# Kernel tuning notes

Hardware: AMD Instinct MI355X
Metric: run time of the kernel (lower is better)

The kernel has to match this reference:

```python
import jax, jax.numpy as jnp
import numpy as np

E = 1024
H = 16
EPS = 1e-5


def setup_inputs() -> dict:
    key = jax.random.key(0)
    ks = jax.random.split(key, 17)
    B, T = 8, 1024
    s = 0.02
    inp = {
        'x': jax.random.normal(ks[0], (B, T, E), dtype=jnp.float32),
        'Wq': jax.random.normal(ks[1], (E, E), dtype=jnp.float32) * s,
        'bq': jnp.zeros((E,), jnp.float32),
        'Wk': jax.random.normal(ks[2], (E, E), dtype=jnp.float32) * s,
        'bk': jnp.zeros((E,), jnp.float32),
        'Wv': jax.random.normal(ks[3], (E, E), dtype=jnp.float32) * s,
        'bv': jnp.zeros((E,), jnp.float32),
        'Wo': jax.random.normal(ks[4], (E, E), dtype=jnp.float32) * s,
        'bo': jnp.zeros((E,), jnp.float32),
        'W1': jax.random.normal(ks[5], (E, 4 * E), dtype=jnp.float32) * s,
        'b1': jnp.zeros((4 * E,), jnp.float32),
        'W2': jax.random.normal(ks[6], (4 * E, E), dtype=jnp.float32) * s,
        'b2': jnp.zeros((E,), jnp.float32),
        'g1': jnp.ones((E,), jnp.float32),
        'be1': jnp.zeros((E,), jnp.float32),
        'g2': jnp.ones((E,), jnp.float32),
        'be2': jnp.zeros((E,), jnp.float32),
    }
    return inp


def _layernorm(x, g, b):
    mu = jnp.mean(x, axis=-1, keepdims=True)
    var = jnp.mean(jnp.square(x - mu), axis=-1, keepdims=True)
    return (x - mu) * jax.lax.rsqrt(var + EPS) * g + b


def _block(x, Wq, bq, Wk, bk, Wv, bv, Wo, bo, W1, b1, W2, b2, g1, be1, g2, be2):
    B, T, Ee = x.shape
    hd = Ee // H
    q = (x @ Wq + bq).reshape(B, T, H, hd).transpose(0, 2, 1, 3)  # (B,H,T,d)
    k = (x @ Wk + bk).reshape(B, T, H, hd).transpose(0, 2, 1, 3)
    v = (x @ Wv + bv).reshape(B, T, H, hd).transpose(0, 2, 1, 3)
    scores = jnp.einsum('bhqd,bhkd->bhqk', q, k) / jnp.sqrt(jnp.float32(hd))
    causal = jnp.tril(jnp.ones((T, T), bool))
    scores = jnp.where(causal, scores, -jnp.inf)
    w = jax.nn.softmax(scores, axis=-1)
    attn = jnp.einsum('bhqk,bhkd->bhqd', w, v)
    attn = attn.transpose(0, 2, 1, 3).reshape(B, T, Ee)
    attn = attn @ Wo + bo  # dropout is identity (p=0 / eval)
    x = _layernorm(x + attn, g1, be1)
    ff = jax.nn.relu(x @ W1 + b1) @ W2 + b2
    x = _layernorm(x + ff, g2, be2)
    return x


def reference(x, Wq, bq, Wk, bk, Wv, bv, Wo, bo, W1, b1, W2, b2, g1, be1, g2, be2):
    return _block(x, Wq, bq, Wk, bk, Wv, bv, Wo, bo, W1, b1, W2, b2, g1, be1, g2, be2)
```

## Files before the change

kernel.cpp:

```cpp
#include <hip/hip_runtime.h>
#include <math.h>

typedef unsigned short u16;
typedef __attribute__((ext_vector_type(8))) short short8;
typedef __attribute__((ext_vector_type(4))) float floatx4;
typedef __attribute__((ext_vector_type(16))) float floatx16;

__device__ __forceinline__ u16 f2bf(float f) {
    unsigned u = __float_as_uint(f);
    unsigned r = u + 0x7fffu + ((u >> 16) & 1u);
    return (u16)(r >> 16);
}

__device__ __forceinline__ void gload16(const u16* g, u16* l) {
    __builtin_amdgcn_global_load_lds((const __attribute__((address_space(1))) void*)g,
                                     (__attribute__((address_space(3))) void*)l, 16, 0, 0);
}

template<int EPI>
__global__ __launch_bounds__(256) void gemm_mfma(
    const u16* __restrict__ A, const u16* __restrict__ Bt,
    const float* __restrict__ bias, const float* __restrict__ bias2,
    const float* __restrict__ bias3, const float* __restrict__ R,
    void* __restrict__ Cout, void* __restrict__ out2, void* __restrict__ out3,
    int M, int N, int K) {
    __shared__ u16 As[128 * 32];
    __shared__ u16 Bs[128 * 32];
    const int tid = threadIdx.x;
    const int wave = tid >> 6, lane = tid & 63;
    const int ar = lane & 31, hl = lane >> 5;
    const int ny = M >> 7, nx = N >> 7;
    const int per = ny * nx;
    const int chunk = blockIdx.x / per, rem = blockIdx.x % per;
    const int nchunks = gridDim.x / per;
    const int by = rem % ny, bx = rem / ny;
    const int m0 = by * 128, n0 = bx * 128;
    const int wm = (wave & 1) * 64, wn = (wave >> 1) * 64;
    const int klen = K / nchunks;
    const int kstart = chunk * klen, kend = kstart + klen;

    floatx16 acc[2][2];
#pragma unroll
    for (int i = 0; i < 2; i++)
#pragma unroll
        for (int j = 0; j < 2; j++)
#pragma unroll
            for (int r = 0; r < 16; r++) acc[i][j][r] = 0.f;

    const int f0 = wave * 128 + lane;

    for (int k0 = kstart; k0 < kend; k0 += 32) {
        __syncthreads();
#pragma unroll
        for (int i = 0; i < 2; i++) {
            int f = f0 + i * 64;
            int row = f >> 2, c = f & 3;
            int cg = c ^ ((row >> 1) & 3);
            gload16(A + (size_t)(m0 + row) * K + k0 + cg * 8, As + f * 8);
            gload16(Bt + (size_t)(n0 + row) * K + k0 + cg * 8, Bs + f * 8);
        }
        __syncthreads();
        short8 af[2][2], bf[2][2];
#pragma unroll
        for (int mt = 0; mt < 2; mt++) {
            int row = wm + mt * 32 + ar;
            int sw = (row >> 1) & 3;
#pragma unroll
            for (int s = 0; s < 2; s++) {
                int ch = (s * 2 + hl) ^ sw;
                af[mt][s] = *(const short8*)(As + row * 32 + ch * 8);
            }
        }
#pragma unroll
        for (int nt = 0; nt < 2; nt++) {
            int row = wn + nt * 32 + ar;
            int sw = (row >> 1) & 3;
#pragma unroll
            for (int s = 0; s < 2; s++) {
                int ch = (s * 2 + hl) ^ sw;
                bf[nt][s] = *(const short8*)(Bs + row * 32 + ch * 8);
            }
        }
#pragma unroll
        for (int s = 0; s < 2; s++)
#pragma unroll
            for (int mt = 0; mt < 2; mt++)
#pragma unroll
                for (int nt = 0; nt < 2; nt++)
                    acc[mt][nt] = __builtin_amdgcn_mfma_f32_32x32x16_bf16(af[mt][s], bf[nt][s], acc[mt][nt], 0, 0, 0);
    }

    const float* bp = bias;
    int sec = 0;
    if (EPI == 4) {
        sec = n0 >> 10;
        bp = sec == 0 ? bias : (sec == 1 ? bias2 : bias3);
    }
    float bv[2];
    if (EPI != 5) {
#pragma unroll
        for (int nt = 0; nt < 2; nt++) {
            int gc = n0 + wn + nt * 32 + ar;
            bv[nt] = bp[EPI == 4 ? (gc & 1023) : gc];
        }
    }

#pragma unroll
    for (int mt = 0; mt < 2; mt++)
#pragma unroll
        for (int nt = 0; nt < 2; nt++) {
            floatx16 a = acc[mt][nt];
            int gc = n0 + wn + nt * 32 + ar;
#pragma unroll
            for (int rg = 0; rg < 4; rg++) {
                int gr0 = m0 + wm + mt * 32 + rg * 8 + hl * 4;
                if (EPI == 1) {
                    u16* C = (u16*)Cout;
#pragma unroll
                    for (int rr = 0; rr < 4; rr++)
                        C[(size_t)(gr0 + rr) * N + gc] = f2bf(fmaxf(a[rg * 4 + rr] + bv[nt], 0.f));
                } else if (EPI == 2) {
                    float* C = (float*)Cout;
#pragma unroll
                    for (int rr = 0; rr < 4; rr++) {
                        size_t idx = (size_t)(gr0 + rr) * N + gc;
                        C[idx] = a[rg * 4 + rr] + bv[nt] + R[idx];
                    }
                } else if (EPI == 5) {
                    float* C = (float*)Cout;
#pragma unroll
                    for (int rr = 0; rr < 4; rr++)
                        unsafeAtomicAdd(&C[(size_t)(gr0 + rr) * N + gc], a[rg * 4 + rr]);
                } else {
                    int nc = gc & 1023;
                    if (sec < 2) {
                        u16* C = (u16*)(sec == 0 ? Cout : out2);
#pragma unroll
                        for (int rr = 0; rr < 4; rr++)
                            C[(size_t)(gr0 + rr) * 1024 + nc] = f2bf(a[rg * 4 + rr] + bv[nt]);
                    } else {
                        u16* C = (u16*)out3;
                        int bb = gr0 >> 10, t0 = gr0 & 1023;
                        size_t idx = ((size_t)(bb * 1024 + nc)) * 1024 + t0;
                        ushort4 u;
                        u.x = f2bf(a[rg * 4 + 0] + bv[nt]); u.y = f2bf(a[rg * 4 + 1] + bv[nt]);
                        u.z = f2bf(a[rg * 4 + 2] + bv[nt]); u.w = f2bf(a[rg * 4 + 3] + bv[nt]);
                        *(ushort4*)(C + idx) = u;
                    }
                }
            }
        }
}

__global__ __launch_bounds__(256) void attn_mfma(
    const u16* __restrict__ q, const u16* __restrict__ k,
    const u16* __restrict__ vT, u16* __restrict__ o) {
    __shared__ u16 Kb[2][64 * 64];
    __shared__ u16 Vb[2][64 * 64];
    __shared__ u16 Pb[4][2][16 * 72];

    const int tid = threadIdx.x;
    const int wave = tid >> 6, lane = tid & 63;
    const int lrow = lane & 15, quad = lane >> 4;
    const int qb = blockIdx.y, bh = blockIdx.x;
    const int b = bh >> 4, h = bh & 15;
    const size_t tokbase = (size_t)b * 1024;
    const int ktmax = qb * 2 + 1;

#pragma unroll
    for (int i = 0; i < 2; i++) {
        int f = wave * 128 + i * 64 + lane;
        int row = f >> 3, c = f & 7, cg = c ^ (row & 7);
        gload16(q + (tokbase + qb * 128 + row) * 1024 + h * 64 + cg * 8, Kb[1] + f * 8);
        gload16(q + (tokbase + qb * 128 + 64 + row) * 1024 + h * 64 + cg * 8, Vb[1] + f * 8);
        gload16(k + (tokbase + row) * 1024 + h * 64 + cg * 8, Kb[0] + f * 8);
        gload16(vT + (tokbase + h * 64 + row) * 1024 + cg * 8, Vb[0] + f * 8);
    }
    asm volatile("s_waitcnt vmcnt(0)" ::: "memory");
    __syncthreads();
    short8 aQ[2][2];
#pragma unroll
    for (int band = 0; band < 2; band++)
#pragma unroll
        for (int ks = 0; ks < 2; ks++) {
            int row = wave * 16 + lrow;
            int pos = (ks * 4 + quad) ^ (lrow & 7);
            const u16* src = band ? Vb[1] : Kb[1];
            aQ[band][ks] = *(const short8*)(src + row * 64 + pos * 8);
        }
    __syncthreads();

    float lp[2][4];
    floatx4 oa[2][4];
#pragma unroll
    for (int bd = 0; bd < 2; bd++)
#pragma unroll
        for (int i = 0; i < 4; i++) { lp[bd][i] = 0.f; oa[bd][i] = {0.f, 0.f, 0.f, 0.f}; }

    for (int kt = 0; kt <= ktmax; kt++) {
        const int cur = kt & 1;
        if (kt < ktmax) {
            const int nxt = cur ^ 1;
#pragma unroll
            for (int i = 0; i < 2; i++) {
                int f = wave * 128 + i * 64 + lane;
                int row = f >> 3, c = f & 7, cg = c ^ (row & 7);
                gload16(k + (tokbase + (kt + 1) * 64 + row) * 1024 + h * 64 + cg * 8, Kb[nxt] + f * 8);
                gload16(vT + (tokbase + h * 64 + row) * 1024 + (kt + 1) * 64 + cg * 8, Vb[nxt] + f * 8);
            }
        }
#pragma unroll
        for (int band = 0; band < 2; band++) {
            const int btile = qb * 2 + band;
            if (kt > btile) continue;
            floatx4 sacc[4];
#pragma unroll
            for (int nt = 0; nt < 4; nt++) sacc[nt] = {0.f, 0.f, 0.f, 0.f};
#pragma unroll
            for (int nt = 0; nt < 4; nt++)
#pragma unroll
                for (int ks = 0; ks < 2; ks++) {
                    int row = nt * 16 + lrow;
                    int pos = (ks * 4 + quad) ^ (lrow & 7);
                    short8 bK = *(const short8*)(Kb[cur] + row * 64 + pos * 8);
                    sacc[nt] = __builtin_amdgcn_mfma_f32_16x16x32_bf16(aQ[band][ks], bK, sacc[nt], 0, 0, 0);
                }
            const bool diag = (kt == btile);
            float p[4][4];
#pragma unroll
            for (int r = 0; r < 4; r++) {
                int qrl = wave * 16 + quad * 4 + r;
#pragma unroll
                for (int nt = 0; nt < 4; nt++) {
                    float e = exp2f(sacc[nt][r] * 0.18033688011112042f);
                    if (diag && (nt * 16 + lrow) > qrl) e = 0.f;
                    p[nt][r] = e;
                    lp[band][r] += e;
                }
            }
            u16* Pw = Pb[wave][band];
#pragma unroll
            for (int nt = 0; nt < 4; nt++)
#pragma unroll
                for (int r = 0; r < 4; r++) {
                    int row = quad * 4 + r, key = nt * 16 + lrow;
                    int pos = ((key >> 3) ^ (row & 7)) * 8 + (key & 7);
                    Pw[row * 72 + pos] = f2bf(p[nt][r]);
                }
            asm volatile("s_waitcnt lgkmcnt(0)" ::: "memory");
            short8 aP[2];
#pragma unroll
            for (int ks = 0; ks < 2; ks++) {
                int pos = (ks * 4 + quad) ^ (lrow & 7);
                aP[ks] = *(const short8*)(Pw + lrow * 72 + pos * 8);
            }
#pragma unroll
            for (int nt = 0; nt < 4; nt++)
#pragma unroll
                for (int ks = 0; ks < 2; ks++) {
                    int row = nt * 16 + lrow;
                    int pos = (ks * 4 + quad) ^ (lrow & 7);
                    short8 bV = *(const short8*)(Vb[cur] + row * 64 + pos * 8);
                    oa[band][nt] = __builtin_amdgcn_mfma_f32_16x16x32_bf16(aP[ks], bV, oa[band][nt], 0, 0, 0);
                }
        }
        __syncthreads();
    }

#pragma unroll
    for (int band = 0; band < 2; band++) {
        float inv[4];
#pragma unroll
        for (int r = 0; r < 4; r++) {
            float l = lp[band][r];
#pragma unroll
            for (int off = 1; off < 16; off <<= 1) l += __shfl_xor(l, off);
            inv[r] = 1.f / l;
        }
#pragma unroll
        for (int nt = 0; nt < 4; nt++)
#pragma unroll
            for (int r = 0; r < 4; r++) {
                int grow = qb * 128 + band * 64 + wave * 16 + quad * 4 + r;
                float v = oa[band][nt][r] * inv[r];
                o[(tokbase + grow) * 1024 + h * 64 + nt * 16 + lrow] = f2bf(v);
            }
    }
}

__device__ __forceinline__ void tconv_tile(const float* __restrict__ W, u16* __restrict__ Wt,
                                           int K, int N, int k0, int n0, int t,
                                           float (*Ts)[33]) {
    const int r = t >> 3, c4 = (t & 7) * 4;
    float4 v = *(const float4*)(W + (size_t)(k0 + r) * N + n0 + c4);
    Ts[c4 + 0][r] = v.x; Ts[c4 + 1][r] = v.y; Ts[c4 + 2][r] = v.z; Ts[c4 + 3][r] = v.w;
    __syncthreads();
    ushort4 u;
    u.x = f2bf(Ts[r][c4 + 0]); u.y = f2bf(Ts[r][c4 + 1]);
    u.z = f2bf(Ts[r][c4 + 2]); u.w = f2bf(Ts[r][c4 + 3]);
    *(ushort4*)(Wt + (size_t)(n0 + r) * K + k0 + c4) = u;
}

__global__ __launch_bounds__(256) void prep_kernel(
    const float* __restrict__ x, const float* __restrict__ Wq, const float* __restrict__ Wk,
    const float* __restrict__ Wv, const float* __restrict__ Wo, const float* __restrict__ W1,
    const float* __restrict__ W2, u16* __restrict__ xb, u16* __restrict__ Wqkvt,
    u16* __restrict__ Wot, u16* __restrict__ W1t, u16* __restrict__ W2t) {
    __shared__ float Ts[32][33];
    const int blk = blockIdx.x, t = threadIdx.x;
    if (blk < 4096) {
        size_t i = ((size_t)blk * 256 + t) * 8;
        float4 a = *(const float4*)(x + i);
        float4 b = *(const float4*)(x + i + 4);
        ushort4 u0, u1;
        u0.x = f2bf(a.x); u0.y = f2bf(a.y); u0.z = f2bf(a.z); u0.w = f2bf(a.w);
        u1.x = f2bf(b.x); u1.y = f2bf(b.y); u1.z = f2bf(b.z); u1.w = f2bf(b.w);
        *(ushort4*)(xb + i) = u0;
        *(ushort4*)(xb + i + 4) = u1;
    } else if (blk < 8192) {
        int s = blk - 4096;
        int which = s >> 10, tt = s & 1023;
        int n0 = (tt & 31) * 32, k0 = (tt >> 5) * 32;
        const float* W = which == 0 ? Wq : which == 1 ? Wk : which == 2 ? Wv : Wo;
        u16* Wt = which == 3 ? Wot : Wqkvt + (size_t)which * 1024 * 1024;
        tconv_tile(W, Wt, 1024, 1024, k0, n0, t, Ts);
    } else if (blk < 12288) {
        int tt = blk - 8192;
        int n0 = (tt & 127) * 32, k0 = (tt >> 7) * 32;
        tconv_tile(W1, W1t, 1024, 4096, k0, n0, t, Ts);
    } else {
        int tt = blk - 12288;
        int n0 = (tt & 31) * 32, k0 = (tt >> 5) * 32;
        tconv_tile(W2, W2t, 4096, 1024, k0, n0, t, Ts);
    }
}

template<int WB, int ADDB>
__global__ __launch_bounds__(256) void ln_kernel(float* __restrict__ x, const float* __restrict__ g,
                                                 const float* __restrict__ bta, u16* __restrict__ xb,
                                                 const float* __restrict__ badd) {
    __shared__ float red[8];
    const int tid = threadIdx.x;
    float* rowp = x + (size_t)blockIdx.x * 1024;
    float4 val = ((const float4*)rowp)[tid];

    float s = val.x + val.y + val.z + val.w;
#pragma unroll
    for (int off = 32; off; off >>= 1) s += __shfl_down(s, off);
    if ((tid & 63) == 0) red[tid >> 6] = s;
    __syncthreads();
    float mu = (red[0] + red[1] + red[2] + red[3]) * (1.f / 1024.f);

    float dx = val.x - mu, dy = val.y - mu, dz = val.z - mu, dw = val.w - mu;
    float sq = dx * dx + dy * dy + dz * dz + dw * dw;
#pragma unroll
    for (int off = 32; off; off >>= 1) sq += __shfl_down(sq, off);
    if ((tid & 63) == 0) red[4 + (tid >> 6)] = sq;
    __syncthreads();
    float var = (red[4] + red[5] + red[6] + red[7]) * (1.f / 1024.f);
    float rs = rsqrtf(var + 1e-5f);

    float4 gv = ((const float4*)g)[tid];
    float4 bv = ((const float4*)bta)[tid];
    float4 ov;
    ov.x = dx * rs * gv.x + bv.x;
    ov.y = dy * rs * gv.y + bv.y;
    ov.z = dz * rs * gv.z + bv.z;
    ov.w = dw * rs * gv.w + bv.w;
    if (WB) {
        u16* rb = xb + (size_t)blockIdx.x * 1024 + tid * 4;
        ushort4 u;
        u.x = f2bf(ov.x); u.y = f2bf(ov.y); u.z = f2bf(ov.z); u.w = f2bf(ov.w);
        *(ushort4*)rb = u;
    }
    if (ADDB) {
        float4 ab = ((const float4*)badd)[tid];
        ov.x += ab.x; ov.y += ab.y; ov.z += ab.z; ov.w += ab.w;
    }
    ((float4*)rowp)[tid] = ov;
}

extern "C" void kernel_launch(void* const* d_in, const int* in_sizes, int n_in,
                              void* d_out, int out_size, void* d_ws, size_t ws_size,
                              hipStream_t stream) {
    const float* x   = (const float*)d_in[0];
    const float* Wq  = (const float*)d_in[1];
    const float* bq  = (const float*)d_in[2];
    const float* Wk  = (const float*)d_in[3];
    const float* bk  = (const float*)d_in[4];
    const float* Wv  = (const float*)d_in[5];
    const float* bv  = (const float*)d_in[6];
    const float* Wo  = (const float*)d_in[7];
    const float* bo  = (const float*)d_in[8];
    const float* W1  = (const float*)d_in[9];
    const float* b1  = (const float*)d_in[10];
    const float* W2  = (const float*)d_in[11];
    const float* b2  = (const float*)d_in[12];
    const float* g1  = (const float*)d_in[13];
    const float* be1 = (const float*)d_in[14];
    const float* g2  = (const float*)d_in[15];
    const float* be2 = (const float*)d_in[16];
    float* out = (float*)d_out;

    u16* w = (u16*)d_ws;
    const size_t SZ_ACT = (size_t)8192 * 1024;
    u16* xb    = w;                  w += SZ_ACT;
    u16* Wqkvt = w;                  w += (size_t)3 * 1024 * 1024;
    u16* Wot   = w;                  w += 1024 * 1024;
    u16* W1t   = w;                  w += (size_t)4096 * 1024;
    u16* W2t   = w;                  w += (size_t)1024 * 4096;
    u16* qb    = w;                  w += SZ_ACT;
    u16* kb    = w;                  w += SZ_ACT;
    u16* vTb   = w;                  w += SZ_ACT;
    u16* attb  = w;                  w += SZ_ACT;
    u16* hbuf  = qb;

    const int M = 8192;
    dim3 blk(256);

    prep_kernel<<<dim3(16384), blk, 0, stream>>>(x, Wq, Wk, Wv, Wo, W1, W2,
                                                 xb, Wqkvt, Wot, W1t, W2t);

    gemm_mfma<4><<<dim3(24 * 64), blk, 0, stream>>>(xb, Wqkvt, bq, bk, bv, nullptr,
                                                    qb, kb, vTb, M, 3072, 1024);
    attn_mfma<<<dim3(128, 8), blk, 0, stream>>>(qb, kb, vTb, attb);
    gemm_mfma<2><<<dim3(8 * 64), blk, 0, stream>>>(attb, Wot, bo, nullptr, nullptr, x,
                                                   out, nullptr, nullptr, M, 1024, 1024);
    ln_kernel<1, 1><<<dim3(8192), blk, 0, stream>>>(out, g1, be1, xb, b2);
    gemm_mfma<1><<<dim3(32 * 64), blk, 0, stream>>>(xb, W1t, b1, nullptr, nullptr, nullptr,
                                                    hbuf, nullptr, nullptr, M, 4096, 1024);
    gemm_mfma<5><<<dim3(2 * 8 * 64), blk, 0, stream>>>(hbuf, W2t, nullptr, nullptr, nullptr, nullptr,
                                                       out, nullptr, nullptr, M, 1024, 4096);
    ln_kernel<0, 0><<<dim3(8192), blk, 0, stream>>>(out, g2, be2, nullptr, nullptr);
}
```

Baseline: 527.5 us.

## Drop split-K atomics, use templated BK with fragment-ordered LDS layout

Makes the GEMM K-tile size a template parameter and replaces the XOR-swizzled LDS layout with a fragment-ordered layout, where each wave loads rows directly in MFMA operand order. The FFN down-projection no longer uses two-way split-K with atomic adds. It now runs a full-K GEMM with bias and residual fused into the epilogue, which removes the bias pre-add trick in the first layernorm. This avoids atomic traffic and the read-modify-write of the output, but it halves the W2 GEMM grid and may change LDS bank-conflict behaviour.

```diff
diff --git a/kernel.cpp b/kernel.cpp
--- a/kernel.cpp
+++ b/kernel.cpp
@@ -17,27 +17,23 @@
                                      (__attribute__((address_space(3))) void*)l, 16, 0, 0);
 }
 
-template<int EPI>
+template<int EPI, int BK>
 __global__ __launch_bounds__(256) void gemm_mfma(
     const u16* __restrict__ A, const u16* __restrict__ Bt,
     const float* __restrict__ bias, const float* __restrict__ bias2,
     const float* __restrict__ bias3, const float* __restrict__ R,
     void* __restrict__ Cout, void* __restrict__ out2, void* __restrict__ out3,
     int M, int N, int K) {
-    __shared__ u16 As[128 * 32];
-    __shared__ u16 Bs[128 * 32];
+    constexpr int S = BK / 16;
+    __shared__ u16 As[128 * BK];
+    __shared__ u16 Bs[128 * BK];
     const int tid = threadIdx.x;
     const int wave = tid >> 6, lane = tid & 63;
     const int ar = lane & 31, hl = lane >> 5;
-    const int ny = M >> 7, nx = N >> 7;
-    const int per = ny * nx;
-    const int chunk = blockIdx.x / per, rem = blockIdx.x % per;
-    const int nchunks = gridDim.x / per;
-    const int by = rem % ny, bx = rem / ny;
+    const int ny = M >> 7;
+    const int by = blockIdx.x % ny, bx = blockIdx.x / ny;
     const int m0 = by * 128, n0 = bx * 128;
     const int wm = (wave & 1) * 64, wn = (wave >> 1) * 64;
-    const int klen = K / nchunks;
-    const int kstart = chunk * klen, kend = kstart + klen;
 
     floatx16 acc[2][2];
 #pragma unroll
@@ -47,42 +43,36 @@
 #pragma unroll
             for (int r = 0; r < 16; r++) acc[i][j][r] = 0.f;
 
-    const int f0 = wave * 128 + lane;
-
-    for (int k0 = kstart; k0 < kend; k0 += 32) {
+    const int srow = wave * 32 + ar;
+
+    for (int k0 = 0; k0 < K; k0 += BK) {
         __syncthreads();
 #pragma unroll
-        for (int i = 0; i < 2; i++) {
-            int f = f0 + i * 64;
-            int row = f >> 2, c = f & 3;
-            int cg = c ^ ((row >> 1) & 3);
-            gload16(A + (size_t)(m0 + row) * K + k0 + cg * 8, As + f * 8);
-            gload16(Bt + (size_t)(n0 + row) * K + k0 + cg * 8, Bs + f * 8);
+        for (int i = 0; i < S; i++) {
+            int kof = k0 + (i * 2 + hl) * 8;
+            u16* dst = (u16*)((wave * S + i) * 1024);
+            gload16(A + (size_t)(m0 + srow) * K + kof, As + (wave * S + i) * 512 + lane * 8);
+            gload16(Bt + (size_t)(n0 + srow) * K + kof, Bs + (wave * S + i) * 512 + lane * 8);
+            (void)dst;
         }
         __syncthreads();
-        short8 af[2][2], bf[2][2];
+        short8 af[2][S], bf[2][S];
 #pragma unroll
         for (int mt = 0; mt < 2; mt++) {
-            int row = wm + mt * 32 + ar;
-            int sw = (row >> 1) & 3;
-#pragma unroll
-            for (int s = 0; s < 2; s++) {
-                int ch = (s * 2 + hl) ^ sw;
-                af[mt][s] = *(const short8*)(As + row * 32 + ch * 8);
-            }
+            int g = (wave & 1) * 2 + mt;
+#pragma unroll
+            for (int s = 0; s < S; s++)
+                af[mt][s] = *(const short8*)(As + (g * S + s) * 512 + lane * 8);
         }
 #pragma unroll
         for (int nt = 0; nt < 2; nt++) {
-            int row = wn + nt * 32 + ar;
-            int sw = (row >> 1) & 3;
-#pragma unroll
-            for (int s = 0; s < 2; s++) {
-                int ch = (s * 2 + hl) ^ sw;
-                bf[nt][s] = *(const short8*)(Bs + row * 32 + ch * 8);
-            }
-        }
-#pragma unroll
-        for (int s = 0; s < 2; s++)
+            int g = (wave >> 1) * 2 + nt;
+#pragma unroll
+            for (int s = 0; s < S; s++)
+                bf[nt][s] = *(const short8*)(Bs + (g * S + s) * 512 + lane * 8);
+        }
+#pragma unroll
+        for (int s = 0; s < S; s++)
 #pragma unroll
             for (int mt = 0; mt < 2; mt++)
 #pragma unroll
@@ -97,12 +87,10 @@
         bp = sec == 0 ? bias : (sec == 1 ? bias2 : bias3);
     }
     float bv[2];
-    if (EPI != 5) {
-#pragma unroll
-        for (int nt = 0; nt < 2; nt++) {
-            int gc = n0 + wn + nt * 32 + ar;
-            bv[nt] = bp[EPI == 4 ? (gc & 1023) : gc];
-        }
+#pragma unroll
+    for (int nt = 0; nt < 2; nt++) {
+        int gc = n0 + wn + nt * 32 + ar;
+        bv[nt] = bp[EPI == 4 ? (gc & 1023) : gc];
     }
 
 #pragma unroll
@@ -126,11 +114,6 @@
                         size_t idx = (size_t)(gr0 + rr) * N + gc;
                         C[idx] = a[rg * 4 + rr] + bv[nt] + R[idx];
                     }
-                } else if (EPI == 5) {
-                    float* C = (float*)Cout;
-#pragma unroll
-                    for (int rr = 0; rr < 4; rr++)
-                        unsafeAtomicAdd(&C[(size_t)(gr0 + rr) * N + gc], a[rg * 4 + rr]);
                 } else {
                     int nc = gc & 1023;
                     if (sec < 2) {
@@ -335,10 +318,9 @@
     }
 }
 
-template<int WB, int ADDB>
+template<int WB>
 __global__ __launch_bounds__(256) void ln_kernel(float* __restrict__ x, const float* __restrict__ g,
-                                                 const float* __restrict__ bta, u16* __restrict__ xb,
-                                                 const float* __restrict__ badd) {
+                                                 const float* __restrict__ bta, u16* __restrict__ xb) {
     __shared__ float red[8];
     const int tid = threadIdx.x;
     float* rowp = x + (size_t)blockIdx.x * 1024;
@@ -367,17 +349,13 @@
     ov.y = dy * rs * gv.y + bv.y;
     ov.z = dz * rs * gv.z + bv.z;
     ov.w = dw * rs * gv.w + bv.w;
+    ((float4*)rowp)[tid] = ov;
     if (WB) {
         u16* rb = xb + (size_t)blockIdx.x * 1024 + tid * 4;
         ushort4 u;
         u.x = f2bf(ov.x); u.y = f2bf(ov.y); u.z = f2bf(ov.z); u.w = f2bf(ov.w);
         *(ushort4*)rb = u;
     }
-    if (ADDB) {
-        float4 ab = ((const float4*)badd)[tid];
-        ov.x += ab.x; ov.y += ab.y; ov.z += ab.z; ov.w += ab.w;
-    }
-    ((float4*)rowp)[tid] = ov;
 }
 
 extern "C" void kernel_launch(void* const* d_in, const int* in_sizes, int n_in,
@@ -421,15 +399,15 @@
     prep_kernel<<<dim3(16384), blk, 0, stream>>>(x, Wq, Wk, Wv, Wo, W1, W2,
                                                  xb, Wqkvt, Wot, W1t, W2t);
 
-    gemm_mfma<4><<<dim3(24 * 64), blk, 0, stream>>>(xb, Wqkvt, bq, bk, bv, nullptr,
-                                                    qb, kb, vTb, M, 3072, 1024);
+    gemm_mfma<4, 32><<<dim3(24 * 64), blk, 0, stream>>>(xb, Wqkvt, bq, bk, bv, nullptr,
+                                                        qb, kb, vTb, M, 3072, 1024);
     attn_mfma<<<dim3(128, 8), blk, 0, stream>>>(qb, kb, vTb, attb);
-    gemm_mfma<2><<<dim3(8 * 64), blk, 0, stream>>>(attb, Wot, bo, nullptr, nullptr, x,
-                                                   out, nullptr, nullptr, M, 1024, 1024);
-    ln_kernel<1, 1><<<dim3(8192), blk, 0, stream>>>(out, g1, be1, xb, b2);
-    gemm_mfma<1><<<dim3(32 * 64), blk, 0, stream>>>(xb, W1t, b1, nullptr, nullptr, nullptr,
-                                                    hbuf, nullptr, nullptr, M, 4096, 1024);
-    gemm_mfma<5><<<dim3(2 * 8 * 64), blk, 0, stream>>>(hbuf, W2t, nullptr, nullptr, nullptr, nullptr,
+    gemm_mfma<2, 64><<<dim3(8 * 64), blk, 0, stream>>>(attb, Wot, bo, nullptr, nullptr, x,
+                                                       out, nullptr, nullptr, M, 1024, 1024);
+    ln_kernel<1><<<dim3(8192), blk, 0, stream>>>(out, g1, be1, xb);
+    gemm_mfma<1, 32><<<dim3(32 * 64), blk, 0, stream>>>(xb, W1t, b1, nullptr, nullptr, nullptr,
+                                                        hbuf, nullptr, nullptr, M, 4096, 1024);
+    gemm_mfma<2, 64><<<dim3(8 * 64), blk, 0, stream>>>(hbuf, W2t, b2, nullptr, nullptr, out,
                                                        out, nullptr, nullptr, M, 1024, 4096);
-    ln_kernel<0, 0><<<dim3(8192), blk, 0, stream>>>(out, g2, be2, nullptr, nullptr);
-}
+    ln_kernel<0><<<dim3(8192), blk, 0, stream>>>(out, g2, be2, nullptr);
+}
```

Result: slower. 641.8 us (+21.7%).
